# Performance work log

Measured on AMD Instinct MI355X. Metric: run time of the kernel, lower is better.

## Reference

```python
import jax, jax.numpy as jnp
import numpy as np

N = 50000        # nodes
E = 800000       # edges (avg degree 16)
IN = 256         # in_feature
HID = 32         # hidden per head
HEADS = 4        # gat_heads
OUT = 64         # out_feature
SLOPE = 0.2      # PyG GATConv default negative_slope


def _gat_layer(x, src, dst, edge_weight, W, a_src, a_dst, b, heads, ch, concat):
    """One GATConv: linear -> per-edge attention logits -> segment softmax over
    incoming edges of each dst node -> weighted scatter-sum. edge_weight scales
    the unnormalized attention (log-space edge weighting, identity at init=1)."""
    n = x.shape[0]
    h = (x @ W).reshape(n, heads, ch)                       # [N,H,C]
    al_s = jnp.einsum('nhc,hc->nh', h, a_src)               # [N,H]
    al_d = jnp.einsum('nhc,hc->nh', h, a_dst)               # [N,H]
    logit = jax.nn.leaky_relu(al_s[src] + al_d[dst], SLOPE) # [E,H]
    m = jax.lax.stop_gradient(jax.ops.segment_max(logit, dst, num_segments=n))
    e = jnp.exp(logit - m[dst]) * edge_weight[:, None]      # [E,H]
    denom = jax.ops.segment_sum(e, dst, num_segments=n)     # [N,H]
    alpha = e / (denom[dst] + 1e-16)                        # [E,H]
    out = jax.ops.segment_sum(h[src] * alpha[..., None], dst, num_segments=n)
    out = out.reshape(n, heads * ch) if concat else out.mean(axis=1)
    return out + b


def setup_inputs() -> dict:
    key = jax.random.key(0)
    ks = jax.random.split(key, 14)
    s = 0.1
    x = jax.random.normal(ks[0], (N, IN), jnp.float32)
    edge_index = jax.random.randint(ks[1], (2, E), 0, N, dtype=jnp.int64)
    edge_weight = jnp.ones((E,), jnp.float32)
    D1 = HEADS * HID
    W1 = jax.random.normal(ks[2], (IN, D1), jnp.float32) * s
    a_src1 = jax.random.normal(ks[3], (HEADS, HID), jnp.float32) * s
    a_dst1 = jax.random.normal(ks[4], (HEADS, HID), jnp.float32) * s
    b1 = jnp.zeros((D1,), jnp.float32)
    W2 = jax.random.normal(ks[5], (D1, D1), jnp.float32) * s
    a_src2 = jax.random.normal(ks[6], (HEADS, HID), jnp.float32) * s
    a_dst2 = jax.random.normal(ks[7], (HEADS, HID), jnp.float32) * s
    b2 = jnp.zeros((D1,), jnp.float32)
    W3 = jax.random.normal(ks[8], (D1, OUT), jnp.float32) * s
    a_src3 = jax.random.normal(ks[9], (1, OUT), jnp.float32) * s
    a_dst3 = jax.random.normal(ks[10], (1, OUT), jnp.float32) * s
    b3 = jnp.zeros((OUT,), jnp.float32)
    return dict(x=x, edge_index=edge_index, edge_weight=edge_weight,
                W1=W1, a_src1=a_src1, a_dst1=a_dst1, b1=b1,
                W2=W2, a_src2=a_src2, a_dst2=a_dst2, b2=b2,
                W3=W3, a_src3=a_src3, a_dst3=a_dst3, b3=b3)


def reference(x, edge_index, edge_weight,
              W1, a_src1, a_dst1, b1,
              W2, a_src2, a_dst2, b2,
              W3, a_src3, a_dst3, b3):
    src, dst = edge_index[0], edge_index[1]
    h = _gat_layer(x, src, dst, edge_weight, W1, a_src1, a_dst1, b1, HEADS, HID, True)
    h = jax.nn.relu(h)  # dropout = identity in eval mode
    h = _gat_layer(h, src, dst, edge_weight, W2, a_src2, a_dst2, b2, HEADS, HID, True)
    h = jax.nn.relu(h)
    out = _gat_layer(h, src, dst, edge_weight, W3, a_src3, a_dst3, b3, 1, OUT, False)
    return out
```

## Files before the change

### kernel.cpp

```cpp
#include <hip/hip_runtime.h>
#include <math.h>

#define NNODES 50000
#define NEDGES 800000

#define BIN_SHIFT 9
#define BIN_W 512
#define NBINS 98
#define CAP 12288
#define ATILE 4096
#define NBINBLK ((NEDGES + ATILE - 1) / ATILE)

typedef _Float16 f16;
typedef __attribute__((ext_vector_type(2))) _Float16 f16x2;
typedef __attribute__((ext_vector_type(4))) _Float16 f16x4;
typedef __attribute__((ext_vector_type(8))) _Float16 f16x8;
typedef __attribute__((ext_vector_type(4))) float f32x4;

__device__ __forceinline__ float leaky02(float v) { return v > 0.f ? v : 0.2f * v; }

__device__ __forceinline__ void wave_lds_fence() {
  __asm__ volatile("s_waitcnt lgkmcnt(0)" ::: "memory");
}


__global__ __launch_bounds__(256) void init_kernel(int* __restrict__ binCursor,
                                                   const float* __restrict__ W1,
                                                   const float* __restrict__ W2,
                                                   const float* __restrict__ W3,
                                                   f16* __restrict__ WT1,
                                                   f16* __restrict__ WT2,
                                                   f16* __restrict__ WT3) {
  int gid = blockIdx.x * 256 + threadIdx.x;
  int stride = gridDim.x * 256;
  if (gid < NBINS) binCursor[gid] = 0;
  for (int i = gid; i < 32768; i += stride) {
    int d = i >> 8, k = i & 255;
    WT1[i] = (f16)W1[k * 128 + d];
  }
  for (int i = gid; i < 16384; i += stride) {
    int d = i >> 7, k = i & 127;
    WT2[i] = (f16)W2[k * 128 + d];
  }
  for (int i = gid; i < 8192; i += stride) {
    int d = i >> 7, k = i & 127;
    WT3[i] = (f16)W3[k * 64 + d];
  }
}


__device__ __forceinline__ void bin_body(int bid,
                                         const int* __restrict__ dst,
                                         const int* __restrict__ src,
                                         const float* __restrict__ ew,
                                         int* __restrict__ binCursor,
                                         int2* __restrict__ binned, int ne) {
  __shared__ int cnt[NBINS];
  __shared__ int gbase[NBINS];
  int tid = threadIdx.x;
  int t0 = bid * ATILE;
  if (tid < NBINS) cnt[tid] = 0;
  __syncthreads();
  int saved[ATILE / 256];
  #pragma unroll
  for (int u = 0; u < ATILE / 256; ++u) {
    int i = t0 + u * 256 + tid;
    int v = 0;
    if (i < ne) {
      int d = dst[i];
      int idx = atomicAdd(&cnt[d >> BIN_SHIFT], 1);
      v = d | (idx << 16);
    }
    saved[u] = v;
  }
  __syncthreads();
  if (tid < NBINS) gbase[tid] = atomicAdd(&binCursor[tid], cnt[tid]);
  __syncthreads();
  #pragma unroll
  for (int u = 0; u < ATILE / 256; ++u) {
    int i = t0 + u * 256 + tid;
    if (i < ne) {
      int v = saved[u];
      int d = v & 0xffff;
      int idx = (int)((unsigned)v >> 16);
      int b = d >> BIN_SHIFT;
      int slot = gbase[b] + idx;
      if (slot < CAP)
        binned[(size_t)b * CAP + slot] =
            make_int2(src[i] | (d << 16), __float_as_int(ew[i]));
    }
  }
}


__global__ __launch_bounds__(256) void build_kernel(const int2* __restrict__ binned,
                                                    const int* __restrict__ binCursor,
                                                    int* __restrict__ offsets,
                                                    int2* __restrict__ edgeSW, int n) {
  __shared__ int sizes[NBINS];
  __shared__ int cnt[BIN_W];
  __shared__ int wsum[4];
  __shared__ int bstartS;
  int tid = threadIdx.x;
  int b = blockIdx.x;
  if (tid < NBINS) sizes[tid] = binCursor[tid];
  cnt[tid] = 0;
  cnt[tid + 256] = 0;
  __syncthreads();
  if (tid == 0) {
    int s = 0;
    for (int k = 0; k < b; ++k) s += (sizes[k] < CAP ? sizes[k] : CAP);
    bstartS = s;
  }
  int mySize = sizes[b];
  if (mySize > CAP) mySize = CAP;
  __syncthreads();
  const int2* mybin = binned + (size_t)b * CAP;
  for (int i = tid; i < mySize; i += 256)
    atomicAdd(&cnt[((unsigned)mybin[i].x >> 16) - b * BIN_W], 1);
  __syncthreads();
  int c0 = cnt[2 * tid], c1 = cnt[2 * tid + 1];
  int s2 = c0 + c1;
  int lane = tid & 63, wid = tid >> 6;
  int incl = s2;
  #pragma unroll
  for (int o = 1; o < 64; o <<= 1) {
    int u = __shfl_up(incl, o, 64);
    if (lane >= o) incl += u;
  }
  if (lane == 63) wsum[wid] = incl;
  __syncthreads();
  if (tid == 0) {
    int r = 0;
    #pragma unroll
    for (int w = 0; w < 4; ++w) { int t = wsum[w]; wsum[w] = r; r += t; }
  }
  __syncthreads();
  int excl0 = bstartS + wsum[wid] + incl - s2;
  int excl1 = excl0 + c0;
  int node0 = b * BIN_W;
  if (node0 + 2 * tid < n)     offsets[node0 + 2 * tid]     = excl0;
  if (node0 + 2 * tid + 1 < n) offsets[node0 + 2 * tid + 1] = excl1;
  if (b == NBINS - 1 && tid == 0) offsets[n] = bstartS + mySize;
  __syncthreads();
  cnt[2 * tid] = excl0;
  cnt[2 * tid + 1] = excl1;
  __syncthreads();
  for (int i = tid; i < mySize; i += 256) {
    int2 r = mybin[i];
    int dloc = (int)((unsigned)r.x >> 16) - b * BIN_W;
    int pos = atomicAdd(&cnt[dloc], 1);
    edgeSW[pos] = make_int2(r.x & 0xffff, r.y);
  }
}


template<typename AT, int BN, int H>
__device__ __forceinline__ void gemm_body(int bid,
                                          const AT* __restrict__ A,
                                          const f16* __restrict__ BT,
                                          f16* __restrict__ C,
                                          const float* __restrict__ a_src,
                                          const float* __restrict__ a_dst,
                                          float* __restrict__ als,
                                          float* __restrict__ ald,
                                          int M, int K) {
  constexpr int BM = 64;
  constexpr int WN = BN / 2;
  constexpr int MT = 2, NT = WN / 16;
  __shared__ f16 As[BM * 72];
  __shared__ f16 Bs[BN * 72];
  int tid = threadIdx.x;
  int lane = tid & 63, wave = tid >> 6;
  int wm = wave & 1, wn = wave >> 1;
  int row0 = bid * BM;
  int quad = lane >> 4, cc = lane & 15;

  f32x4 acc[MT][NT];
  #pragma unroll
  for (int mt = 0; mt < MT; ++mt)
    #pragma unroll
    for (int nt = 0; nt < NT; ++nt)
      acc[mt][nt] = (f32x4){0.f, 0.f, 0.f, 0.f};

  for (int k0 = 0; k0 < K; k0 += 64) {
    __syncthreads();
    if constexpr (sizeof(AT) == 4) {
      #pragma unroll
      for (int i = 0; i < 4; ++i) {
        int r = i * 16 + (tid >> 4);
        int kc = (tid & 15) * 4;
        float4 av = make_float4(0.f, 0.f, 0.f, 0.f);
        if (row0 + r < M) av = *(const float4*)&A[(size_t)(row0 + r) * K + k0 + kc];
        *(f16x4*)&As[r * 72 + kc] = (f16x4){(f16)av.x, (f16)av.y, (f16)av.z, (f16)av.w};
      }
    } else {
      #pragma unroll
      for (int i = 0; i < 2; ++i) {
        int r = i * 32 + (tid >> 3);
        int kc = (tid & 7) * 8;
        f16x8 hv = {0, 0, 0, 0, 0, 0, 0, 0};
        if (row0 + r < M) hv = *(const f16x8*)&A[(size_t)(row0 + r) * K + k0 + kc];
        *(f16x8*)&As[r * 72 + kc] = hv;
      }
    }
    #pragma unroll
    for (int i = 0; i < BN / 32; ++i) {
      int d = i * 32 + (tid >> 3);
      int kc = (tid & 7) * 8;
      *(f16x8*)&Bs[d * 72 + kc] = *(const f16x8*)&BT[(size_t)d * K + k0 + kc];
    }
    __syncthreads();
    #pragma unroll
    for (int ki = 0; ki < 2; ++ki) {
      f16x8 a[MT], b[NT];
      #pragma unroll
      for (int mt = 0; mt < MT; ++mt)
        a[mt] = *(const f16x8*)&As[(wm * 32 + mt * 16 + cc) * 72 + ki * 32 + quad * 8];
      #pragma unroll
      for (int nt = 0; nt < NT; ++nt)
        b[nt] = *(const f16x8*)&Bs[(wn * WN + nt * 16 + cc) * 72 + ki * 32 + quad * 8];
      #pragma unroll
      for (int mt = 0; mt < MT; ++mt)
        #pragma unroll
        for (int nt = 0; nt < NT; ++nt)
          acc[mt][nt] = __builtin_amdgcn_mfma_f32_16x16x32_f16(a[mt], b[nt], acc[mt][nt], 0, 0, 0);
    }
  }

  float asv[NT], adv[NT];
  #pragma unroll
  for (int nt = 0; nt < NT; ++nt) {
    int ch = wn * WN + nt * 16 + cc;
    asv[nt] = a_src[ch];
    adv[nt] = a_dst[ch];
  }

  #pragma unroll
  for (int mt = 0; mt < MT; ++mt)
    #pragma unroll
    for (int v = 0; v < 4; ++v) {
      int row = row0 + wm * 32 + mt * 16 + quad * 4 + v;
      if (row < M) {
        #pragma unroll
        for (int nt = 0; nt < NT; ++nt)
          C[(size_t)row * BN + wn * WN + nt * 16 + cc] = (f16)acc[mt][nt][v];
      }
      float s0 = acc[mt][0][v] * asv[0] + acc[mt][1][v] * asv[1];
      float s1 = acc[mt][2][v] * asv[2] + acc[mt][3][v] * asv[3];
      float d0 = acc[mt][0][v] * adv[0] + acc[mt][1][v] * adv[1];
      float d1 = acc[mt][2][v] * adv[2] + acc[mt][3][v] * adv[3];
      #pragma unroll
      for (int o = 1; o < 16; o <<= 1) {
        s0 += __shfl_xor(s0, o);
        s1 += __shfl_xor(s1, o);
        d0 += __shfl_xor(d0, o);
        d1 += __shfl_xor(d1, o);
      }
      if (cc == 0 && row < M) {
        *(float2*)&als[row * 4 + 2 * wn] = make_float2(s0, s1);
        *(float2*)&ald[row * 4 + 2 * wn] = make_float2(d0, d1);
      }
    }
}


__global__ __launch_bounds__(256) void fused_front_kernel(const int* __restrict__ dst,
                                                          const int* __restrict__ src,
                                                          const float* __restrict__ ew,
                                                          int* __restrict__ binCursor,
                                                          int2* __restrict__ binned, int ne,
                                                          const float* __restrict__ A,
                                                          const f16* __restrict__ BT,
                                                          f16* __restrict__ C,
                                                          const float* __restrict__ a_src,
                                                          const float* __restrict__ a_dst,
                                                          float* __restrict__ als,
                                                          float* __restrict__ ald,
                                                          int M, int K) {
  if (blockIdx.x < NBINBLK)
    bin_body(blockIdx.x, dst, src, ew, binCursor, binned, ne);
  else
    gemm_body<float, 128, 4>(blockIdx.x - NBINBLK, A, BT, C, a_src, a_dst, als, ald, M, K);
}


template<int BN, int H>
__global__ __launch_bounds__(512) void fused_aggemm_kernel(
    const f16* __restrict__ hg,
    const float* __restrict__ als_i,
    const float* __restrict__ ald_i,
    const int* __restrict__ offsets,
    const int2* __restrict__ edgeSW,
    const float* __restrict__ bias,
    const f16* __restrict__ BT,
    f16* __restrict__ C,
    const float* __restrict__ a_src,
    const float* __restrict__ a_dst,
    float* __restrict__ als_o,
    float* __restrict__ ald_o,
    int n_nodes) {
  constexpr int K = 128;
  constexpr int BM = 64;
  constexpr int WN = BN / 4;
  constexpr int MT = 2, NT = WN / 16;
  __shared__ f16 As[BM * 136];
  __shared__ f16 Bs[BN * 72];
  __shared__ int   swS[16][32];
  __shared__ float swW[16][4][36];
  __shared__ float redS[2][4][32], redD[2][4][32];

  int tid = threadIdx.x;
  int hw = tid >> 5, hl = tid & 31;
  int row0 = blockIdx.x * BM;
  int h2 = hl >> 4, l16 = hl & 15;
  int head = l16 >> 2;

  for (int p = 0; p < 4; ++p) {
    int node = row0 + p * 16 + hw;
    bool valid = node < n_nodes;
    int nodeC = valid ? node : n_nodes - 1;
    int start = offsets[nodeC], end = offsets[nodeC + 1];
    int deg = valid ? end - start : 0;

    float4 aldv = *(const float4*)&ald_i[nodeC * 4];

    int s0 = 0; float wgt0 = 0.f;
    float v0 = 0.f, v1 = 0.f, v2 = 0.f, v3 = 0.f;
    float m0 = -INFINITY, m1 = -INFINITY, m2 = -INFINITY, m3 = -INFINITY;
    if (hl < deg) {
      int2 e = edgeSW[start + hl];
      s0 = e.x;
      wgt0 = __int_as_float(e.y);
      float4 a4 = *(const float4*)&als_i[s0 * 4];
      v0 = leaky02(a4.x + aldv.x); m0 = v0;
      v1 = leaky02(a4.y + aldv.y); m1 = v1;
      v2 = leaky02(a4.z + aldv.z); m2 = v2;
      v3 = leaky02(a4.w + aldv.w); m3 = v3;
    }
    for (int j = start + 32 + hl; j < end; j += 32) {
      int2 e = edgeSW[j];
      float4 a4 = *(const float4*)&als_i[e.x * 4];
      m0 = fmaxf(m0, leaky02(a4.x + aldv.x));
      m1 = fmaxf(m1, leaky02(a4.y + aldv.y));
      m2 = fmaxf(m2, leaky02(a4.z + aldv.z));
      m3 = fmaxf(m3, leaky02(a4.w + aldv.w));
    }
    #pragma unroll
    for (int o = 16; o > 0; o >>= 1) {
      m0 = fmaxf(m0, __shfl_xor(m0, o, 32));
      m1 = fmaxf(m1, __shfl_xor(m1, o, 32));
      m2 = fmaxf(m2, __shfl_xor(m2, o, 32));
      m3 = fmaxf(m3, __shfl_xor(m3, o, 32));
    }
    float w0 = 0.f, w1 = 0.f, w2 = 0.f, w3 = 0.f;
    if (hl < deg) {
      w0 = __expf(v0 - m0) * wgt0;
      w1 = __expf(v1 - m1) * wgt0;
      w2 = __expf(v2 - m2) * wgt0;
      w3 = __expf(v3 - m3) * wgt0;
    }
    swS[hw][hl] = s0;
    swW[hw][0][hl] = w0;
    swW[hw][1][hl] = w1;
    swW[hw][2][hl] = w2;
    swW[hw][3][hl] = w3;
    wave_lds_fence();

    float acc0 = 0.f, acc1 = 0.f, acc2 = 0.f, acc3 = 0.f;
    float acc4 = 0.f, acc5 = 0.f, acc6 = 0.f, acc7 = 0.f;
    float dd = 0.f;
    int cn = deg < 32 ? deg : 32;
    int nb = (cn + 15) >> 4;
    for (int b = 0; b < nb; ++b) {
      int j0 = b * 16 + h2 * 8;
      int4   sa = *(const int4*)&swS[hw][j0];
      int4   sb = *(const int4*)&swS[hw][j0 + 4];
      float4 wa = *(const float4*)&swW[hw][head][j0];
      float4 wb = *(const float4*)&swW[hw][head][j0 + 4];
      int   sj[8] = {sa.x, sa.y, sa.z, sa.w, sb.x, sb.y, sb.z, sb.w};
      float wj[8] = {wa.x, wa.y, wa.z, wa.w, wb.x, wb.y, wb.z, wb.w};
      f16x8 hv[8];
      #pragma unroll
      for (int u = 0; u < 8; ++u)
        hv[u] = *(const f16x8*)&hg[(size_t)sj[u] * 128 + 8 * l16];
      #pragma unroll
      for (int u = 0; u < 8; ++u) {
        dd += wj[u];
        acc0 += wj[u] * (float)hv[u][0];
        acc1 += wj[u] * (float)hv[u][1];
        acc2 += wj[u] * (float)hv[u][2];
        acc3 += wj[u] * (float)hv[u][3];
        acc4 += wj[u] * (float)hv[u][4];
        acc5 += wj[u] * (float)hv[u][5];
        acc6 += wj[u] * (float)hv[u][6];
        acc7 += wj[u] * (float)hv[u][7];
      }
    }
    for (int base = start + 32; base < end; base += 32) {
      int cnt = end - base; if (cnt > 32) cnt = 32;
      int st = 0; float u0 = 0.f, u1 = 0.f, u2 = 0.f, u3 = 0.f;
      if (hl < cnt) {
        int2 e = edgeSW[base + hl];
        st = e.x;
        float wg = __int_as_float(e.y);
        float4 a4 = *(const float4*)&als_i[st * 4];
        u0 = __expf(leaky02(a4.x + aldv.x) - m0) * wg;
        u1 = __expf(leaky02(a4.y + aldv.y) - m1) * wg;
        u2 = __expf(leaky02(a4.z + aldv.z) - m2) * wg;
        u3 = __expf(leaky02(a4.w + aldv.w) - m3) * wg;
      }
      for (int jj = h2; jj < cnt; jj += 2) {
        int sjr = __shfl(st, jj, 32);
        float t0 = __shfl(u0, jj, 32), t1 = __shfl(u1, jj, 32);
        float t2 = __shfl(u2, jj, 32), t3 = __shfl(u3, jj, 32);
        float wr = head == 0 ? t0 : head == 1 ? t1 : head == 2 ? t2 : t3;
        f16x8 hv = *(const f16x8*)&hg[(size_t)sjr * 128 + 8 * l16];
        dd += wr;
        acc0 += wr * (float)hv[0];
        acc1 += wr * (float)hv[1];
        acc2 += wr * (float)hv[2];
        acc3 += wr * (float)hv[3];
        acc4 += wr * (float)hv[4];
        acc5 += wr * (float)hv[5];
        acc6 += wr * (float)hv[6];
        acc7 += wr * (float)hv[7];
      }
    }

    acc0 += __shfl_xor(acc0, 16, 32);
    acc1 += __shfl_xor(acc1, 16, 32);
    acc2 += __shfl_xor(acc2, 16, 32);
    acc3 += __shfl_xor(acc3, 16, 32);
    acc4 += __shfl_xor(acc4, 16, 32);
    acc5 += __shfl_xor(acc5, 16, 32);
    acc6 += __shfl_xor(acc6, 16, 32);
    acc7 += __shfl_xor(acc7, 16, 32);
    dd   += __shfl_xor(dd, 16, 32);

    if (h2 == 0) {
      f16x8 val = {0, 0, 0, 0, 0, 0, 0, 0};
      if (valid) {
        float inv = 1.f / (dd + 1e-16f);
        float4 bv0 = *(const float4*)&bias[8 * l16];
        float4 bv1 = *(const float4*)&bias[8 * l16 + 4];
        float o0 = fmaxf(acc0 * inv + bv0.x, 0.f), o1 = fmaxf(acc1 * inv + bv0.y, 0.f);
        float o2 = fmaxf(acc2 * inv + bv0.z, 0.f), o3 = fmaxf(acc3 * inv + bv0.w, 0.f);
        float o4 = fmaxf(acc4 * inv + bv1.x, 0.f), o5 = fmaxf(acc5 * inv + bv1.y, 0.f);
        float o6 = fmaxf(acc6 * inv + bv1.z, 0.f), o7 = fmaxf(acc7 * inv + bv1.w, 0.f);
        val = (f16x8){(f16)o0, (f16)o1, (f16)o2, (f16)o3, (f16)o4, (f16)o5, (f16)o6, (f16)o7};
      }
      *(f16x8*)&As[(p * 16 + hw) * 136 + 8 * l16] = val;
    }
  }

  int lane = tid & 63, wave = tid >> 6;
  int wm = wave & 1, wn = wave >> 1;
  int quad = lane >> 4, cc = lane & 15;

  f32x4 acc[MT][NT];
  #pragma unroll
  for (int mt = 0; mt < MT; ++mt)
    #pragma unroll
    for (int nt = 0; nt < NT; ++nt)
      acc[mt][nt] = (f32x4){0.f, 0.f, 0.f, 0.f};

  for (int k0 = 0; k0 < K; k0 += 64) {
    __syncthreads();
    #pragma unroll
    for (int i = 0; i < (BN * 8) / 512; ++i) {
      int idx = i * 512 + tid;
      int d = idx >> 3, kc = (idx & 7) * 8;
      *(f16x8*)&Bs[d * 72 + kc] = *(const f16x8*)&BT[(size_t)d * K + k0 + kc];
    }
    __syncthreads();
    #pragma unroll
    for (int ki = 0; ki < 2; ++ki) {
      f16x8 a[MT], b[NT];
      #pragma unroll
      for (int mt = 0; mt < MT; ++mt)
        a[mt] = *(const f16x8*)&As[(wm * 32 + mt * 16 + cc) * 136 + k0 + ki * 32 + quad * 8];
      #pragma unroll
      for (int nt = 0; nt < NT; ++nt)
        b[nt] = *(const f16x8*)&Bs[(wn * WN + nt * 16 + cc) * 72 + ki * 32 + quad * 8];
      #pragma unroll
      for (int mt = 0; mt < MT; ++mt)
        #pragma unroll
        for (int nt = 0; nt < NT; ++nt)
          acc[mt][nt] = __builtin_amdgcn_mfma_f32_16x16x32_f16(a[mt], b[nt], acc[mt][nt], 0, 0, 0);
    }
  }

  float asv[NT], adv[NT];
  #pragma unroll
  for (int nt = 0; nt < NT; ++nt) {
    int ch = wn * WN + nt * 16 + cc;
    asv[nt] = a_src[ch];
    adv[nt] = a_dst[ch];
  }

  #pragma unroll
  for (int mt = 0; mt < MT; ++mt)
    #pragma unroll
    for (int v = 0; v < 4; ++v) {
      int row = row0 + wm * 32 + mt * 16 + quad * 4 + v;
      if (row < n_nodes) {
        #pragma unroll
        for (int nt = 0; nt < NT; ++nt)
          C[(size_t)row * BN + wn * WN + nt * 16 + cc] = (f16)acc[mt][nt][v];
      }
      if constexpr (H == 4) {
        float s0 = acc[mt][0][v] * asv[0] + acc[mt][1][v] * asv[1];
        float d0 = acc[mt][0][v] * adv[0] + acc[mt][1][v] * adv[1];
        #pragma unroll
        for (int o = 1; o < 16; o <<= 1) {
          s0 += __shfl_xor(s0, o);
          d0 += __shfl_xor(d0, o);
        }
        if (cc == 0 && row < n_nodes) {
          als_o[row * 4 + wn] = s0;
          ald_o[row * 4 + wn] = d0;
        }
      } else {
        float s0 = acc[mt][0][v] * asv[0];
        float d0 = acc[mt][0][v] * adv[0];
        #pragma unroll
        for (int o = 1; o < 16; o <<= 1) {
          s0 += __shfl_xor(s0, o);
          d0 += __shfl_xor(d0, o);
        }
        int r = mt * 16 + quad * 4 + v;
        if (cc == 0) { redS[wm][wn][r] = s0; redD[wm][wn][r] = d0; }
      }
    }
  if constexpr (H == 1) {
    __syncthreads();
    #pragma unroll
    for (int mt = 0; mt < MT; ++mt)
      #pragma unroll
      for (int v = 0; v < 4; ++v) {
        int row = row0 + wm * 32 + mt * 16 + quad * 4 + v;
        int r = mt * 16 + quad * 4 + v;
        if (wn == 0 && cc == 0 && row < n_nodes) {
          als_o[row] = redS[wm][0][r] + redS[wm][1][r] + redS[wm][2][r] + redS[wm][3][r];
          ald_o[row] = redD[wm][0][r] + redD[wm][1][r] + redD[wm][2][r] + redD[wm][3][r];
        }
      }
  }
}

__global__ __launch_bounds__(256) void aggregate1_kernel(const f16* __restrict__ h16,
                                                         const float* __restrict__ als,
                                                         const float* __restrict__ ald,
                                                         const int* __restrict__ offsets,
                                                         const int2* __restrict__ edgeSW,
                                                         const float* __restrict__ bias,
                                                         float* __restrict__ out, int n_nodes) {
  __shared__ int   s1s[8][32];
  __shared__ float w1s[8][32];
  int hw = threadIdx.x >> 5;
  int hl = threadIdx.x & 31;
  int node = blockIdx.x * 8 + hw;
  bool valid = node < n_nodes;
  int nodeC = valid ? node : n_nodes - 1;
  int start = offsets[nodeC], end = offsets[nodeC + 1];
  int deg = valid ? end - start : 0;

  float ald0 = ald[nodeC];
  int s0 = 0; float wgt0 = 0.f, v0 = 0.f, m0 = -INFINITY;
  if (hl < deg) {
    int2 e = edgeSW[start + hl];
    s0 = e.x;
    wgt0 = __int_as_float(e.y);
    v0 = leaky02(als[s0] + ald0);
    m0 = v0;
  }
  for (int j = start + 32 + hl; j < end; j += 32) {
    int2 e = edgeSW[j];
    m0 = fmaxf(m0, leaky02(als[e.x] + ald0));
  }
  #pragma unroll
  for (int o = 16; o > 0; o >>= 1) m0 = fmaxf(m0, __shfl_xor(m0, o, 32));

  float w0 = (hl < deg) ? __expf(v0 - m0) * wgt0 : 0.f;
  s1s[hw][hl] = s0;
  w1s[hw][hl] = w0;
  wave_lds_fence();

  int h2 = hl >> 4, l16 = hl & 15;
  float aX = 0.f, aY = 0.f, aZ = 0.f, aW = 0.f, dd = 0.f;
  int cn = deg < 32 ? deg : 32;
  int nb = (cn + 15) >> 4;
  for (int b = 0; b < nb; ++b) {
    int j0 = b * 16 + h2 * 8;
    int4   sa = *(const int4*)&s1s[hw][j0];
    int4   sb = *(const int4*)&s1s[hw][j0 + 4];
    float4 wa = *(const float4*)&w1s[hw][j0];
    float4 wb = *(const float4*)&w1s[hw][j0 + 4];
    int   sj[8] = {sa.x, sa.y, sa.z, sa.w, sb.x, sb.y, sb.z, sb.w};
    float wj[8] = {wa.x, wa.y, wa.z, wa.w, wb.x, wb.y, wb.z, wb.w};
    f16x4 hv[8];
    #pragma unroll
    for (int u = 0; u < 8; ++u)
      hv[u] = *(const f16x4*)&h16[(size_t)sj[u] * 64 + 4 * l16];
    #pragma unroll
    for (int u = 0; u < 8; ++u) {
      dd += wj[u];
      aX += wj[u] * (float)hv[u][0];
      aY += wj[u] * (float)hv[u][1];
      aZ += wj[u] * (float)hv[u][2];
      aW += wj[u] * (float)hv[u][3];
    }
  }
  for (int base = start + 32; base < end; base += 32) {
    int cnt = end - base; if (cnt > 32) cnt = 32;
    int st = 0; float u0 = 0.f;
    if (hl < cnt) {
      int2 e = edgeSW[base + hl];
      st = e.x;
      u0 = __expf(leaky02(als[st] + ald0) - m0) * __int_as_float(e.y);
    }
    for (int jj = h2; jj < cnt; jj += 2) {
      int sjr = __shfl(st, jj, 32);
      float wr = __shfl(u0, jj, 32);
      f16x4 hv = *(const f16x4*)&h16[(size_t)sjr * 64 + 4 * l16];
      dd += wr;
      aX += wr * (float)hv[0];
      aY += wr * (float)hv[1];
      aZ += wr * (float)hv[2];
      aW += wr * (float)hv[3];
    }
  }

  aX += __shfl_xor(aX, 16, 32);
  aY += __shfl_xor(aY, 16, 32);
  aZ += __shfl_xor(aZ, 16, 32);
  aW += __shfl_xor(aW, 16, 32);
  dd += __shfl_xor(dd, 16, 32);

  if (valid && h2 == 0) {
    float inv = 1.f / (dd + 1e-16f);
    float4 bv = *(const float4*)&bias[4 * l16];
    float4 ov = make_float4(aX * inv + bv.x, aY * inv + bv.y,
                            aZ * inv + bv.z, aW * inv + bv.w);
    *(float4*)&out[(size_t)node * 64 + 4 * l16] = ov;
  }
}


extern "C" void kernel_launch(void* const* d_in, const int* in_sizes, int n_in,
                              void* d_out, int out_size, void* d_ws, size_t ws_size,
                              hipStream_t stream) {
  const int N = NNODES, E = NEDGES;
  const float* x   = (const float*)d_in[0];
  const int*   ei  = (const int*)d_in[1];
  const float* ew  = (const float*)d_in[2];
  const float* W1  = (const float*)d_in[3];
  const float* as1 = (const float*)d_in[4];
  const float* ad1 = (const float*)d_in[5];
  const float* b1  = (const float*)d_in[6];
  const float* W2  = (const float*)d_in[7];
  const float* as2 = (const float*)d_in[8];
  const float* ad2 = (const float*)d_in[9];
  const float* b2  = (const float*)d_in[10];
  const float* W3  = (const float*)d_in[11];
  const float* as3 = (const float*)d_in[12];
  const float* ad3 = (const float*)d_in[13];
  const float* b3  = (const float*)d_in[14];
  const int* src = ei;
  const int* dst = ei + E;

  uint8_t* p = (uint8_t*)d_ws;
  auto carve = [&](size_t bytes) {
    void* r = (void*)p;
    p += (bytes + 255) & ~(size_t)255;
    return r;
  };
  int*   binCursor = (int*)carve((size_t)NBINS * 4);
  int*   offsets   = (int*)carve((size_t)(N + 1) * 4);
  int2*  binned    = (int2*)carve((size_t)NBINS * CAP * 8);
  int2*  edgeSW    = (int2*)carve((size_t)E * 8);
  float* als1      = (float*)carve((size_t)N * 4 * 4);
  float* ald1      = (float*)carve((size_t)N * 4 * 4);
  float* als2      = (float*)carve((size_t)N * 4 * 4);
  float* ald2      = (float*)carve((size_t)N * 4 * 4);
  float* als3      = (float*)carve((size_t)N * 4);
  float* ald3      = (float*)carve((size_t)N * 4);
  f16*   hA16      = (f16*)carve((size_t)N * 128 * 2);
  f16*   hB16      = (f16*)carve((size_t)N * 128 * 2);
  f16*   hC16      = (f16*)carve((size_t)N * 64 * 2);
  f16*   WT1       = (f16*)carve((size_t)256 * 128 * 2);
  f16*   WT2       = (f16*)carve((size_t)128 * 128 * 2);
  f16*   WT3       = (f16*)carve((size_t)128 * 64 * 2);

  int gemmGrid = (N + 63) / 64;
  int aggGrid = (N + 7) / 8;

  init_kernel<<<128, 256, 0, stream>>>(binCursor, W1, W2, W3, WT1, WT2, WT3);

  fused_front_kernel<<<NBINBLK + gemmGrid, 256, 0, stream>>>(
      dst, src, ew, binCursor, binned, E,
      x, WT1, hA16, as1, ad1, als1, ald1, N, 256);
  build_kernel<<<NBINS, 256, 0, stream>>>(binned, binCursor, offsets, edgeSW, N);

  fused_aggemm_kernel<128, 4><<<gemmGrid, 512, 0, stream>>>(
      hA16, als1, ald1, offsets, edgeSW, b1,
      WT2, hB16, as2, ad2, als2, ald2, N);
  fused_aggemm_kernel<64, 1><<<gemmGrid, 512, 0, stream>>>(
      hB16, als2, ald2, offsets, edgeSW, b2,
      WT3, hC16, as3, ad3, als3, ald3, N);
  aggregate1_kernel<<<aggGrid, 256, 0, stream>>>(hC16, als3, ald3, offsets, edgeSW,
                                                 b3, (float*)d_out, N);
}
```

Measured before the change: 267.8 us.

## Prefetch next node's edge and attention data; alias Bs with edge staging LDS

Hoists the offset and destination-logit loads for all four node passes ahead of the aggregation loop. It also software-pipelines the first edge record and source-logit gather for the next node while the current node's neighbour aggregation runs. The Bs tile and the swS/swW edge staging buffers now share one union LDS region, which lowers shared memory per block and may raise occupancy. This relies on the GEMM phase's __syncthreads separating the two uses, and it adds register pressure from the prefetched values held across iterations.

Result: no change. 270.7 us (+1.1%).

```diff
diff --git a/kernel.cpp b/kernel.cpp
--- a/kernel.cpp
+++ b/kernel.cpp
@@ -304,11 +304,17 @@
   constexpr int BM = 64;
   constexpr int WN = BN / 4;
   constexpr int MT = 2, NT = WN / 16;
+  constexpr int BS_BYTES = BN * 72 * 2;
+  constexpr int SW_BYTES = 16 * 32 * 4 + 16 * 4 * 36 * 4;
+  constexpr int UNI_BYTES = BS_BYTES > SW_BYTES ? BS_BYTES : SW_BYTES;
+
   __shared__ f16 As[BM * 136];
-  __shared__ f16 Bs[BN * 72];
-  __shared__ int   swS[16][32];
-  __shared__ float swW[16][4][36];
+  __shared__ __align__(16) char uni[UNI_BYTES];
   __shared__ float redS[2][4][32], redD[2][4][32];
+
+  f16* Bs = (f16*)uni;
+  int   (*swS)[32]     = (int(*)[32])uni;
+  float (*swW)[4][36]  = (float(*)[4][36])(uni + 16 * 32 * 4);
 
   int tid = threadIdx.x;
   int hw = tid >> 5, hl = tid & 31;
@@ -316,29 +322,41 @@
   int h2 = hl >> 4, l16 = hl & 15;
   int head = l16 >> 2;
 
+  int startA[4], degA[4];
+  float4 aldvA[4];
+  #pragma unroll
   for (int p = 0; p < 4; ++p) {
     int node = row0 + p * 16 + hw;
     bool valid = node < n_nodes;
     int nodeC = valid ? node : n_nodes - 1;
-    int start = offsets[nodeC], end = offsets[nodeC + 1];
-    int deg = valid ? end - start : 0;
-
-    float4 aldv = *(const float4*)&ald_i[nodeC * 4];
-
-    int s0 = 0; float wgt0 = 0.f;
+    startA[p] = offsets[nodeC];
+    int e = offsets[nodeC + 1];
+    degA[p] = valid ? e - startA[p] : 0;
+    aldvA[p] = *(const float4*)&ald_i[nodeC * 4];
+  }
+  int2 eC = make_int2(0, 0);
+  if (hl < degA[0]) eC = edgeSW[startA[0] + hl];
+  float4 a4C = *(const float4*)&als_i[eC.x * 4];
+
+  #pragma unroll
+  for (int p = 0; p < 4; ++p) {
+    int start = startA[p], deg = degA[p];
+    bool valid = (row0 + p * 16 + hw) < n_nodes;
+    float4 aldv = aldvA[p];
+
+    int s0 = eC.x;
+    float wgt0 = __int_as_float(eC.y);
     float v0 = 0.f, v1 = 0.f, v2 = 0.f, v3 = 0.f;
     float m0 = -INFINITY, m1 = -INFINITY, m2 = -INFINITY, m3 = -INFINITY;
     if (hl < deg) {
-      int2 e = edgeSW[start + hl];
-      s0 = e.x;
-      wgt0 = __int_as_float(e.y);
-      float4 a4 = *(const float4*)&als_i[s0 * 4];
-      v0 = leaky02(a4.x + aldv.x); m0 = v0;
-      v1 = leaky02(a4.y + aldv.y); m1 = v1;
-      v2 = leaky02(a4.z + aldv.z); m2 = v2;
-      v3 = leaky02(a4.w + aldv.w); m3 = v3;
-    }
-    for (int j = start + 32 + hl; j < end; j += 32) {
+      v0 = leaky02(a4C.x + aldv.x); m0 = v0;
+      v1 = leaky02(a4C.y + aldv.y); m1 = v1;
+      v2 = leaky02(a4C.z + aldv.z); m2 = v2;
+      v3 = leaky02(a4C.w + aldv.w); m3 = v3;
+    } else {
+      s0 = 0; wgt0 = 0.f;
+    }
+    for (int j = start + 32 + hl; j < start + deg; j += 32) {
       int2 e = edgeSW[j];
       float4 a4 = *(const float4*)&als_i[e.x * 4];
       m0 = fmaxf(m0, leaky02(a4.x + aldv.x));
@@ -397,8 +415,11 @@
         acc7 += wj[u] * (float)hv[u][7];
       }
     }
-    for (int base = start + 32; base < end; base += 32) {
-      int cnt = end - base; if (cnt > 32) cnt = 32;
+    int2 eN = make_int2(0, 0);
+    if (p < 3 && hl < degA[p + 1]) eN = edgeSW[startA[p + 1] + hl];
+
+    for (int base = start + 32; base < start + deg; base += 32) {
+      int cnt = start + deg - base; if (cnt > 32) cnt = 32;
       int st = 0; float u0 = 0.f, u1 = 0.f, u2 = 0.f, u3 = 0.f;
       if (hl < cnt) {
         int2 e = edgeSW[base + hl];
@@ -428,6 +449,8 @@
       }
     }
 
+    float4 a4N = *(const float4*)&als_i[eN.x * 4];
+
     acc0 += __shfl_xor(acc0, 16, 32);
     acc1 += __shfl_xor(acc1, 16, 32);
     acc2 += __shfl_xor(acc2, 16, 32);
@@ -452,6 +475,8 @@
       }
       *(f16x8*)&As[(p * 16 + hw) * 136 + 8 * l16] = val;
     }
+    eC = eN;
+    a4C = a4N;
   }
 
   int lane = tid & 63, wave = tid >> 6;
```
